# Optimization experiments

Measured on AMD Instinct MI355X. Metric: run time of the kernel, lower is better.

Reference implementation:

```python
import jax, jax.numpy as jnp
import numpy as np

B = 4194304
N_BINS = 201  # rounded values -10.0 .. 10.0 step 0.1


def setup_inputs() -> dict:
    key = jax.random.key(0)
    k1, k2, k3 = jax.random.split(key, 3)
    inp = jax.random.normal(k1, (B, 5), dtype=jnp.float32)
    tgt = jax.random.normal(k2, (B, 5), dtype=jnp.float32)
    # per-channel sorted histogram bin centers, rounded to 1 decimal
    row = (jnp.arange(N_BINS, dtype=jnp.float32) - 100.0) / 10.0  # [-10.0, 10.0]
    steps = jnp.tile(row[None, :], (5, 1))  # [5, N_BINS]
    counts = jax.random.randint(k3, (5, N_BINS), 0, 100000, dtype=jnp.int32)
    return {"input": inp, "target": tgt, "steps": steps, "counts": counts}


def _channel_weights(r, st, cn, tot):
    # r: [B] rounded inputs for one channel; st: [N_BINS] sorted steps; cn: [N_BINS]
    idx = jnp.clip(jnp.searchsorted(st, r), 0, st.shape[0] - 1)
    match = jnp.abs(st[idx] - r) < 1e-4  # membership test (rounded to 1 decimal)
    return jnp.where(match, 1.0 - cn[idx] / tot, 1.0)


def reference(input, target, steps, counts):
    counts_f = counts.astype(jnp.float32)
    totals = counts_f.sum(axis=1)  # [5]
    rounded = jnp.round(input * 10.0) / 10.0  # round to 1 decimal, half-to-even
    # vmap over the 5 channels (column axis of input)
    weights = jax.vmap(_channel_weights, in_axes=(1, 0, 0, 0), out_axes=1)(
        rounded, steps, counts_f, totals
    )  # [B, 5]
    # in torch the weights are built via torch.tensor(...) -> no grad flow
    weights = jax.lax.stop_gradient(weights)
    loss = weights * (input - target) ** 2
    return loss.mean()
```

## Files before the change

### kernel.cpp

```cpp
#include <hip/hip_runtime.h>

#define NBINS 201
#define NCH 5
#define NTOT (NCH * NBINS)
#define B_ELEMS (4194304 * 5)
#define NVEC (B_ELEMS / 4)

__global__ __launch_bounds__(256) void dwmse_kernel(
    const float* __restrict__ inp,
    const float* __restrict__ tgt,
    const int*  __restrict__ counts,
    float* __restrict__ out)
{
    __shared__ int   s_c[NTOT];
    __shared__ float s_w[NTOT];
    __shared__ float s_tot[NCH];
    __shared__ float s_part[4];

    for (int i = threadIdx.x; i < NTOT; i += blockDim.x)
        s_c[i] = counts[i];
    __syncthreads();

    if (threadIdx.x < NCH) {
        long long t = 0;
        const int* row = &s_c[threadIdx.x * NBINS];
        for (int i = 0; i < NBINS; ++i) t += row[i];
        s_tot[threadIdx.x] = (float)t;
    }
    __syncthreads();

    for (int i = threadIdx.x; i < NTOT; i += blockDim.x) {
        int c = i / NBINS;
        s_w[i] = 1.0f - (float)s_c[i] / s_tot[c];
    }
    __syncthreads();

    float acc = 0.0f;
    int g      = blockIdx.x * blockDim.x + threadIdx.x;
    int stride = gridDim.x * blockDim.x;
    const float4* in4 = (const float4*)inp;
    const float4* tg4 = (const float4*)tgt;
    for (int v = g; v < NVEC; v += stride) {
        float4 a = in4[v];
        float4 b = tg4[v];
        int base = v * 4;
        int c0   = base % 5;
        float xs[4] = {a.x, a.y, a.z, a.w};
        float ts[4] = {b.x, b.y, b.z, b.w};
        #pragma unroll
        for (int j = 0; j < 4; ++j) {
            int c = c0 + j; if (c >= NCH) c -= NCH;
            float x  = xs[j];
            float kf = rintf(x * 10.0f);
            float w  = 1.0f;
            if (kf >= -100.0f && kf <= 100.0f) {
                int ki = (int)kf;
                w = s_w[c * NBINS + (ki + 100)];
            }
            float d = x - ts[j];
            acc = fmaf(w * d, d, acc);
        }
    }

    #pragma unroll
    for (int o = 32; o > 0; o >>= 1)
        acc += __shfl_down(acc, o, 64);
    int lane = threadIdx.x & 63;
    int wid  = threadIdx.x >> 6;
    if (lane == 0) s_part[wid] = acc;
    __syncthreads();
    if (threadIdx.x == 0) {
        float s = (s_part[0] + s_part[1]) + (s_part[2] + s_part[3]);
        atomicAdd(out, s * (1.0f / (float)B_ELEMS));
    }
}

extern "C" void kernel_launch(void* const* d_in, const int* in_sizes, int n_in,
                              void* d_out, int out_size, void* d_ws, size_t ws_size,
                              hipStream_t stream) {
    const float* inp    = (const float*)d_in[0];
    const float* tgt    = (const float*)d_in[1];
    const int*   counts = (const int*)d_in[3];

    hipMemsetAsync(d_out, 0, sizeof(float), stream);

    const int block = 256;
    const int grid  = 2048;
    dwmse_kernel<<<grid, block, 0, stream>>>(inp, tgt, counts, (float*)d_out);
}
```

Baseline: 201.1 us.

## Replace grid-stride loop with fixed 8-way unrolled batched float4 loads per thread

The grid-stride loop is replaced by a fixed mapping in which each thread issues 8 input and 8 target float4 loads up front, strided by the total thread count, and then processes them. The grid grows to exactly cover the data, 2560 blocks instead of 2048. Because the stride in elements is a multiple of 5, the per-lane channel bin offsets are computed once per thread instead of per element. The aim is more memory-level parallelism and less loop overhead. The cost is higher register pressure, and every block still repeats the shared-memory weight-table setup.

After: 196.9 us. 2.1% less time.

```diff
diff --git a/kernel.cpp b/kernel.cpp
--- a/kernel.cpp
+++ b/kernel.cpp
@@ -5,8 +5,12 @@
 #define NTOT (NCH * NBINS)
 #define B_ELEMS (4194304 * 5)
 #define NVEC (B_ELEMS / 4)
+#define UNROLL 8
+#define NTHREADS (NVEC / UNROLL)
+#define BLOCK 256
+#define GRID (NTHREADS / BLOCK)
 
-__global__ __launch_bounds__(256) void dwmse_kernel(
+__global__ __launch_bounds__(BLOCK) void dwmse_kernel(
     const float* __restrict__ inp,
     const float* __restrict__ tgt,
     const int*  __restrict__ counts,
@@ -17,7 +21,7 @@
     __shared__ float s_tot[NCH];
     __shared__ float s_part[4];
 
-    for (int i = threadIdx.x; i < NTOT; i += blockDim.x)
+    for (int i = threadIdx.x; i < NTOT; i += BLOCK)
         s_c[i] = counts[i];
     __syncthreads();
 
@@ -29,34 +33,42 @@
     }
     __syncthreads();
 
-    for (int i = threadIdx.x; i < NTOT; i += blockDim.x) {
+    for (int i = threadIdx.x; i < NTOT; i += BLOCK) {
         int c = i / NBINS;
         s_w[i] = 1.0f - (float)s_c[i] / s_tot[c];
     }
     __syncthreads();
 
-    float acc = 0.0f;
-    int g      = blockIdx.x * blockDim.x + threadIdx.x;
-    int stride = gridDim.x * blockDim.x;
+    const int g = blockIdx.x * BLOCK + threadIdx.x;
     const float4* in4 = (const float4*)inp;
     const float4* tg4 = (const float4*)tgt;
-    for (int v = g; v < NVEC; v += stride) {
-        float4 a = in4[v];
-        float4 b = tg4[v];
-        int base = v * 4;
-        int c0   = base % 5;
-        float xs[4] = {a.x, a.y, a.z, a.w};
-        float ts[4] = {b.x, b.y, b.z, b.w};
+
+    float4 a[UNROLL], b[UNROLL];
+    #pragma unroll
+    for (int t = 0; t < UNROLL; ++t) a[t] = in4[g + t * NTHREADS];
+    #pragma unroll
+    for (int t = 0; t < UNROLL; ++t) b[t] = tg4[g + t * NTHREADS];
+
+    const int c0 = (4 * g) % 5;
+    int rb[4];
+    #pragma unroll
+    for (int j = 0; j < 4; ++j) {
+        int c = c0 + j; if (c >= NCH) c -= NCH;
+        rb[j] = c * NBINS + 100;
+    }
+
+    float acc = 0.0f;
+    #pragma unroll
+    for (int t = 0; t < UNROLL; ++t) {
+        float xs[4] = {a[t].x, a[t].y, a[t].z, a[t].w};
+        float ts[4] = {b[t].x, b[t].y, b[t].z, b[t].w};
         #pragma unroll
         for (int j = 0; j < 4; ++j) {
-            int c = c0 + j; if (c >= NCH) c -= NCH;
             float x  = xs[j];
             float kf = rintf(x * 10.0f);
             float w  = 1.0f;
-            if (kf >= -100.0f && kf <= 100.0f) {
-                int ki = (int)kf;
-                w = s_w[c * NBINS + (ki + 100)];
-            }
+            if (kf >= -100.0f && kf <= 100.0f)
+                w = s_w[rb[j] + (int)kf];
             float d = x - ts[j];
             acc = fmaf(w * d, d, acc);
         }
@@ -83,8 +95,5 @@
     const int*   counts = (const int*)d_in[3];
 
     hipMemsetAsync(d_out, 0, sizeof(float), stream);
-
-    const int block = 256;
-    const int grid  = 2048;
-    dwmse_kernel<<<grid, block, 0, stream>>>(inp, tgt, counts, (float*)d_out);
+    dwmse_kernel<<<GRID, BLOCK, 0, stream>>>(inp, tgt, counts, (float*)d_out);
 }
```
